# Kernel optimization log

Measured on AMD Instinct MI355X. Metric: run time of the kernel, lower is better.

## Reference

```python
import jax, jax.numpy as jnp
import numpy as np

ALPHA = 1.702
LIMIT = 7.0
BLOCK = 32  # mxfp4 block size (values per scale)

# fp4 e2m1 lookup table, indexed by 4-bit code (sign in high bit)
FP4_LUT = jnp.array([0.0, 0.5, 1.0, 1.5, 2.0, 3.0, 4.0, 6.0,
                     -0.0, -0.5, -1.0, -1.5, -2.0, -3.0, -4.0, -6.0],
                    dtype=jnp.float32)


def dequant_mxfp4(blocks, scales):
    # blocks: [E, R, C//2] int byte values (two fp4 nibbles per byte, low nibble first)
    # scales: [E, R, C//32] e8m0 exponents; value = 2^(scale - 127)
    E, R, _ = blocks.shape
    nb = scales.shape[-1]
    lo = blocks & 0xF
    hi = (blocks >> 4) & 0xF
    vals = jnp.stack([FP4_LUT[lo], FP4_LUT[hi]], axis=-1)  # [E,R,C//2,2]
    vals = vals.reshape(E, R, nb, BLOCK)
    scale = jnp.exp2((scales - 127).astype(jnp.float32))   # [E,R,nb]
    return (vals * scale[..., None]).reshape(E, R, nb * BLOCK)  # [E,R,C]


def setup_inputs() -> dict:
    key = jax.random.key(0)
    ks = jax.random.split(key, 12)
    T, E, H, I = 1024, 8, 1024, 1024
    inp = {
        'hidden_states': jax.random.normal(ks[0], (T, H), dtype=jnp.float32),
        'router_logits': jax.random.normal(ks[1], (T, E), dtype=jnp.float32),
        'gate_proj_blocks': jax.random.randint(ks[2], (E, I, H // 2), 0, 256, dtype=jnp.int32),
        'gate_proj_scales': jax.random.randint(ks[3], (E, I, H // BLOCK), 121, 130, dtype=jnp.int32),
        'gate_proj_bias': jax.random.normal(ks[4], (E, I), dtype=jnp.float32) * 0.02,
        'up_proj_blocks': jax.random.randint(ks[5], (E, I, H // 2), 0, 256, dtype=jnp.int32),
        'up_proj_scales': jax.random.randint(ks[6], (E, I, H // BLOCK), 121, 130, dtype=jnp.int32),
        'up_proj_bias': jax.random.normal(ks[7], (E, I), dtype=jnp.float32) * 0.02,
        'down_proj_blocks': jax.random.randint(ks[8], (E, H, I // 2), 0, 256, dtype=jnp.int32),
        'down_proj_scales': jax.random.randint(ks[9], (E, H, I // BLOCK), 121, 130, dtype=jnp.int32),
        'down_proj_bias': jax.random.normal(ks[10], (E, H), dtype=jnp.float32) * 0.02,
        'k': 2,
    }
    return inp


def reference(hidden_states, router_logits, gate_proj_blocks, gate_proj_scales,
              gate_proj_bias, up_proj_blocks, up_proj_scales, up_proj_bias,
              down_proj_blocks, down_proj_scales, down_proj_bias, k):
    T, H = hidden_states.shape
    E = router_logits.shape[-1]
    # --- top-k routing: softmax over the selected logits, scattered to [T,E] ---
    top_vals, top_idx = jax.lax.top_k(router_logits, k)        # [T,k]
    top_w = jax.nn.softmax(top_vals, axis=-1)                   # [T,k]
    route = jnp.zeros((T, E), dtype=hidden_states.dtype)
    route = route.at[jnp.arange(T)[:, None], top_idx].add(top_w)  # [T,E]
    # --- dequantize mxfp4 expert weights ---
    gate_w = dequant_mxfp4(gate_proj_blocks, gate_proj_scales)  # [E,I,H]
    up_w = dequant_mxfp4(up_proj_blocks, up_proj_scales)        # [E,I,H]
    down_w = dequant_mxfp4(down_proj_blocks, down_proj_scales)  # [E,H,I]
    # --- GLU expert FFN (GPT-OSS variant) ---
    gate = jnp.einsum('th,eih->tei', hidden_states, gate_w) + gate_proj_bias[None]
    up = jnp.einsum('th,eih->tei', hidden_states, up_w) + up_proj_bias[None]
    gate = jnp.minimum(gate, LIMIT)
    up = jnp.clip(up, -LIMIT, LIMIT)
    glu = gate * jax.nn.sigmoid(gate * ALPHA)
    act = (up + 1.0) * glu                                       # [T,E,I]
    # fold routing weight in before the down projection, then sum over experts
    act = act * route[:, :, None]
    out = jnp.einsum('tei,ehi->th', act, down_w) + route @ down_proj_bias  # [T,H]
    return out
```

## Files before the change

### kernel.cpp

```cpp
#include <hip/hip_runtime.h>
#include <cstdint>
#include <cstddef>

typedef __bf16 bf16x8 __attribute__((ext_vector_type(8)));
typedef __bf16 bf16x2 __attribute__((ext_vector_type(2)));
typedef float f32x16 __attribute__((ext_vector_type(16)));
typedef unsigned short u16x2 __attribute__((ext_vector_type(2)));

constexpr int HH = 1024;
constexpr int II = 1024;
constexpr int KMAX = 2;
constexpr int EMAX = 8;
constexpr int GU_TILES = 40;
constexpr int DN_TILES = 40;
constexpr float FALPHA = 1.702f;
constexpr float FLIMIT = 7.0f;

#if __has_builtin(__builtin_amdgcn_cvt_scalef32_pk_bf16_fp4)
#define USE_CVT 1
#else
#define USE_CVT 0
#endif

#define SCHED0() __builtin_amdgcn_sched_barrier(0)

__device__ __forceinline__ unsigned pk_add16(unsigned a, unsigned b) {
  u16x2 x, y;
  __builtin_memcpy(&x, &a, 4); __builtin_memcpy(&y, &b, 4);
  u16x2 r = x + y;
  unsigned o; __builtin_memcpy(&o, &r, 4); return o;
}
__device__ __forceinline__ int4 decode_chunk(int4 raw, unsigned addk) {
  unsigned p = (unsigned)raw.x | ((unsigned)raw.y << 8) |
               ((unsigned)raw.z << 16) | ((unsigned)raw.w << 24);
  unsigned q = p >> 4;
  unsigned me = p & 0x07070707u, mo = q & 0x07070707u;
  unsigned se = p & 0x08080808u, so = q & 0x08080808u;
  unsigned hiE = __builtin_amdgcn_perm(0x40404040u, 0x3F3F3F14u, me) | (se << 4);
  unsigned hiO = __builtin_amdgcn_perm(0x40404040u, 0x3F3F3F14u, mo) | (so << 4);
  unsigned loE = __builtin_amdgcn_perm(0xC0804000u, 0xC0800000u, me);
  unsigned loO = __builtin_amdgcn_perm(0xC0804000u, 0xC0800000u, mo);
  int4 out;
  out.x = (int)pk_add16(__builtin_amdgcn_perm(hiE, loE, 0x05010400u), addk);
  out.y = (int)pk_add16(__builtin_amdgcn_perm(hiE, loE, 0x07030602u), addk);
  out.z = (int)pk_add16(__builtin_amdgcn_perm(hiO, loO, 0x05010400u), addk);
  out.w = (int)pk_add16(__builtin_amdgcn_perm(hiO, loO, 0x07030602u), addk);
  return out;
}
__device__ __forceinline__ unsigned make_addk(int s) {
  int k = s - 127;
  unsigned t = ((unsigned)(k << 7)) & 0xFFFFu;
  return t | (t << 16);
}

__device__ __forceinline__ bf16x8 decode_frag(int4 raw, int s) {
#if USE_CVT
  unsigned t0 = __builtin_amdgcn_perm((unsigned)raw.y, (unsigned)raw.x, 0x00000400u);
  unsigned t1 = __builtin_amdgcn_perm((unsigned)raw.w, (unsigned)raw.z, 0x00000400u);
  unsigned p  = __builtin_amdgcn_perm(t1, t0, 0x05040100u);
  float scf = __uint_as_float((unsigned)s << 23);
  bf16x2 a = __builtin_amdgcn_cvt_scalef32_pk_bf16_fp4(p, scf, 0);
  bf16x2 b = __builtin_amdgcn_cvt_scalef32_pk_bf16_fp4(p, scf, 1);
  bf16x2 c = __builtin_amdgcn_cvt_scalef32_pk_bf16_fp4(p, scf, 2);
  bf16x2 d = __builtin_amdgcn_cvt_scalef32_pk_bf16_fp4(p, scf, 3);
  bf16x8 r;
  r[0]=a[0]; r[1]=a[1]; r[2]=b[0]; r[3]=b[1]; r[4]=c[0]; r[5]=c[1]; r[6]=d[0]; r[7]=d[1];
  return r;
#else
  int4 d4 = decode_chunk(raw, make_addk(s));
  bf16x8 r; __builtin_memcpy(&r, &d4, 16);
  return r;
#endif
}

__device__ __forceinline__ void gll16(const void* g, void* l) {
  __builtin_amdgcn_global_load_lds(
      (const __attribute__((address_space(1))) void*)g,
      (__attribute__((address_space(3))) void*)l, 16, 0, 0);
}

__device__ __forceinline__ int xcd_swz(int wg, int nwg) {
  int q = nwg >> 3, r = nwg & 7;
  int xcd = wg & 7, pos = wg >> 3;
  return (xcd < r ? xcd * (q + 1) : r * (q + 1) + (xcd - r) * q) + pos;
}

__global__ __launch_bounds__(1024) void prep_convert(
    const float* __restrict__ logits, const int* __restrict__ dk, int T, int E,
    float* __restrict__ route, float* __restrict__ tw,
    int* __restrict__ lists, int* __restrict__ counts,
    int* __restrict__ tabGU, int* __restrict__ tabDN,
    const float* __restrict__ hs, __bf16* __restrict__ hsb, int n8) {
  if ((int)blockIdx.x < (int)gridDim.x - 1) {
    int g = blockIdx.x * 1024 + threadIdx.x;
    if (g < n8) {
      const float4* p = (const float4*)hs + (size_t)g * 2;
      float4 a = p[0], b = p[1];
      bf16x8 r;
#if USE_CVT
      r[0] = (__bf16)a.x; r[1] = (__bf16)a.y; r[2] = (__bf16)a.z; r[3] = (__bf16)a.w;
      r[4] = (__bf16)b.x; r[5] = (__bf16)b.y; r[6] = (__bf16)b.z; r[7] = (__bf16)b.w;
#else
      r[0] = (__bf16)a.x; r[1] = (__bf16)a.z; r[2] = (__bf16)b.x; r[3] = (__bf16)b.z;
      r[4] = (__bf16)a.y; r[5] = (__bf16)a.w; r[6] = (__bf16)b.y; r[7] = (__bf16)b.w;
#endif
      *(bf16x8*)(hsb + (size_t)g * 8) = r;
    }
    return;
  }
  __shared__ unsigned char s_ti[1024];
  __shared__ int s_cnt[EMAX];
  int t = threadIdx.x;
  int kk = *dk; if (kk > KMAX) kk = KMAX; if (kk < 1) kk = 1;
  int EE = E > EMAX ? EMAX : E;
  if (t < T) {
    float v[EMAX]; bool used[EMAX];
    for (int e = 0; e < EE; ++e) { v[e] = logits[t * E + e]; used[e] = false; route[t * E + e] = 0.f; }
    float tv[KMAX]; int ti[KMAX];
    for (int j = 0; j < kk; ++j) {
      float best = -3.4e38f; int bi = 0;
      for (int e = 0; e < EE; ++e) if (!used[e] && v[e] > best) { best = v[e]; bi = e; }
      used[bi] = true; tv[j] = best; ti[j] = bi;
    }
    float mx = tv[0], ssum = 0.f, wj[KMAX];
    for (int j = 0; j < kk; ++j) { wj[j] = __expf(tv[j] - mx); ssum += wj[j]; }
    for (int j = 0; j < kk; ++j) {
      float wv = wj[j] / ssum;
      route[t * E + ti[j]] = wv;
      tw[t * kk + j] = wv;
    }
    s_ti[t] = (unsigned char)(ti[0] | ((kk > 1 ? ti[1] : 0xF) << 4));
  } else if (t < 1024) {
    s_ti[t] = 0xFF;
  }
  __syncthreads();
  int w = t >> 6, lane = t & 63;
  if (w < EE) {
    int e = w, cnt = 0;
    for (int base = 0; base < T; base += 64) {
      int tt = base + lane;
      int j = -1;
      if (tt < T) {
        int packed = s_ti[tt];
        if ((packed & 0xF) == e) j = 0;
        else if ((packed >> 4) == e) j = 1;
      }
      unsigned long long m = __ballot(j >= 0);
      if (j >= 0) {
        int pre = __popcll(m & ((1ull << lane) - 1ull));
        lists[e * T + cnt + pre] = (tt << 3) | j;
      }
      cnt += __popcll(m);
    }
    if (lane == 0) { counts[e] = cnt; s_cnt[e] = cnt; }
  }
  __syncthreads();
  if (t == 0) {
    int g = 0, d = 0;
    for (int e = 0; e < EE; ++e) {
      int c = s_cnt[e];
      for (int m = 0; m * 64 < c && g < GU_TILES; ++m) tabGU[g++] = (e << 16) | m;
      for (int m = 0; m * 64 < c && d < DN_TILES; ++m) tabDN[d++] = (e << 16) | m;
    }
    for (; g < GU_TILES; ++g) tabGU[g] = -1;
    for (; d < DN_TILES; ++d) tabDN[d] = -1;
  }
}

__global__ __launch_bounds__(128, 2) void gemm_gate_up(
    const __bf16* __restrict__ hsb,
    const int* __restrict__ gblk, const int* __restrict__ gscl, const float* __restrict__ gbias,
    const int* __restrict__ ublk, const int* __restrict__ uscl, const float* __restrict__ ubias,
    const int* __restrict__ lists, const int* __restrict__ counts,
    const float* __restrict__ tw, const int* __restrict__ dk,
    const int* __restrict__ tab,
    __bf16* __restrict__ act, int T)
{
  int lin = xcd_swz(blockIdx.x, GU_TILES * (II / 32));
  int ntile = lin / GU_TILES, xt = lin % GU_TILES;
  int te = tab[xt];
  if (te < 0) return;
  int e = te >> 16, mtile = te & 0xFFFF;
  int cnt = counts[e];
  int n_valid = cnt - mtile * 64;
  if (n_valid <= 0) return;
  if (n_valid > 64) n_valid = 64;
  int kk = *dk; if (kk > KMAX) kk = KMAX; if (kk < 1) kk = 1;
  int ibase = ntile * 32;

  __shared__ int s_tok[64];
  __shared__ __attribute__((aligned(16))) char Abuf[2][8192];
  __shared__ __attribute__((aligned(16))) char Bbuf[2][8192];
  __shared__ __attribute__((aligned(8))) unsigned short sS[64][36];

  int tid = threadIdx.x;
  if (tid < 64) {
    int idx = mtile * 64 + tid;
    s_tok[tid] = lists[e * T + (idx < cnt ? idx : mtile * 64)];
  }
  __syncthreads();

  int lane = tid & 63, w = tid >> 6;
  int l31 = lane & 31, kg2 = lane >> 5;
  int sub = lane >> 3, cL = lane & 7;
  int cA = cL ^ (sub & 7);

  const char* aSrc[4];
  #pragma unroll
  for (int q = 0; q < 4; ++q) {
    int row = w * 32 + q * 8 + sub;
    int tok = s_tok[row] >> 3;
    aSrc[q] = (const char*)hsb + (size_t)tok * (HH * 2) + (size_t)cA * 16;
  }
  const char* bSrc[4];
  #pragma unroll
  for (int q = 0; q < 4; ++q) {
    int row = w * 32 + q * 8 + sub;
    int mat = (row >> 4) & 1;
    int i = ibase + ((row >> 5) << 4) + (row & 15);
    const int* base = mat ? ublk : gblk;
    bSrc[q] = (const char*)(base + ((size_t)e * II + i) * (HH / 2)) + (size_t)cA * 16;
  }

  int4 sv4[4];
  #pragma unroll
  for (int rep = 0; rep < 4; ++rep) {
    int idx = tid + rep * 128;
    int row = idx >> 3, c4 = idx & 7;
    int mat = (row >> 4) & 1;
    int i = ibase + ((row >> 5) << 4) + (row & 15);
    const int* sbase = mat ? uscl : gscl;
    sv4[rep] = *((const int4*)(sbase + ((size_t)e * II + i) * 32) + c4);
  }
  asm volatile("s_waitcnt vmcnt(0)" ::: "memory");
  SCHED0();
  #pragma unroll
  for (int rep = 0; rep < 4; ++rep) {
    int idx = tid + rep * 128;
    int row = idx >> 3, c4 = idx & 7;
    unsigned short* dst = &sS[row][c4 * 4];
    dst[0] = (unsigned short)sv4[rep].x; dst[1] = (unsigned short)sv4[rep].y;
    dst[2] = (unsigned short)sv4[rep].z; dst[3] = (unsigned short)sv4[rep].w;
  }
  #pragma unroll
  for (int q = 0; q < 4; ++q) {
    gll16(aSrc[q], Abuf[0] + (w * 32 + q * 8) * 128);
    gll16(bSrc[q], Bbuf[0] + (w * 32 + q * 8) * 128);
  }
  #pragma unroll
  for (int q = 0; q < 4; ++q) {
    gll16(aSrc[q] + 128, Abuf[1] + (w * 32 + q * 8) * 128);
    gll16(bSrc[q] + 128, Bbuf[1] + (w * 32 + q * 8) * 128);
  }
  asm volatile("s_waitcnt vmcnt(8)" ::: "memory");
  asm volatile("s_waitcnt lgkmcnt(0)" ::: "memory");
  SCHED0();
  __builtin_amdgcn_s_barrier();
  SCHED0();

  f32x16 acc0 = (f32x16)0.f, acc1 = (f32x16)0.f;
  int brow = w * 32 + l31;

  constexpr int NK = HH / 64;
  #pragma unroll 1
  for (int t = 0; t < NK; ++t) {
    const char* Ac = Abuf[t & 1];
    const char* Bc = Bbuf[t & 1];
    unsigned sv = *(const unsigned*)((const char*)sS + brow * 72 + t * 4);
    #pragma unroll
    for (int s = 0; s < 4; ++s) {
      int kc = kg2 + 2 * s;
      int4 rawb = *(const int4*)(Bc + brow * 128 + ((kc ^ (brow & 7)) << 4));
      bf16x8 bb = decode_frag(rawb, (s >> 1) ? (int)(sv >> 16) : (int)(sv & 0xFFFF));
      bf16x8 a0 = *(const bf16x8*)(Ac + l31 * 128 + ((kc ^ (l31 & 7)) << 4));
      int m1 = l31 + 32;
      bf16x8 a1 = *(const bf16x8*)(Ac + m1 * 128 + ((kc ^ (m1 & 7)) << 4));
      acc0 = __builtin_amdgcn_mfma_f32_32x32x16_bf16(a0, bb, acc0, 0, 0, 0);
      acc1 = __builtin_amdgcn_mfma_f32_32x32x16_bf16(a1, bb, acc1, 0, 0, 0);
    }
    asm volatile("s_waitcnt lgkmcnt(0)" ::: "memory");
    SCHED0();
    __builtin_amdgcn_s_barrier();
    SCHED0();
    if (t + 2 < NK) {
      char* An = Abuf[t & 1];
      char* Bn = Bbuf[t & 1];
      #pragma unroll
      for (int q = 0; q < 4; ++q) {
        gll16(aSrc[q] + (t + 2) * 128, An + (w * 32 + q * 8) * 128);
        gll16(bSrc[q] + (t + 2) * 128, Bn + (w * 32 + q * 8) * 128);
      }
      asm volatile("s_waitcnt vmcnt(8)" ::: "memory");
    } else {
      asm volatile("s_waitcnt vmcnt(0)" ::: "memory");
    }
    SCHED0();
    __builtin_amdgcn_s_barrier();
    SCHED0();
  }

  {
    bool isGate = (l31 & 16) == 0;
    int i_log = ibase + w * 16 + (l31 & 15);
    float gb = gbias[e * II + i_log], ub = ubias[e * II + i_log];
#if USE_CVT
    int i_st = i_log;
#else
    int i_st = (i_log & ~7) | ((i_log & 1) << 2) | ((i_log & 7) >> 1);
#endif
    #pragma unroll
    for (int r = 0; r < 16; ++r) {
      float gv = acc0[r];
      float ov = __shfl_xor(gv, 16);
      int row = (r & 3) + 8 * (r >> 2) + 4 * kg2;
      if (isGate && row < n_valid) {
        int entry = s_tok[row];
        int t2 = entry >> 3, j = entry & 7;
        float wv = tw[t2 * kk + j];
        float g = fminf(gv + gb, FLIMIT);
        float u = fminf(fmaxf(ov + ub, -FLIMIT), FLIMIT);
        float glu = g / (1.f + __expf(-FALPHA * g));
        act[((size_t)t2 * kk + j) * II + i_st] = (__bf16)((u + 1.f) * glu * wv);
      }
    }
    #pragma unroll
    for (int r = 0; r < 16; ++r) {
      float gv = acc1[r];
      float ov = __shfl_xor(gv, 16);
      int row = (r & 3) + 8 * (r >> 2) + 4 * kg2 + 32;
      if (isGate && row < n_valid) {
        int entry = s_tok[row];
        int t2 = entry >> 3, j = entry & 7;
        float wv = tw[t2 * kk + j];
        float g = fminf(gv + gb, FLIMIT);
        float u = fminf(fmaxf(ov + ub, -FLIMIT), FLIMIT);
        float glu = g / (1.f + __expf(-FALPHA * g));
        act[((size_t)t2 * kk + j) * II + i_st] = (__bf16)((u + 1.f) * glu * wv);
      }
    }
  }
}

__global__ __launch_bounds__(128, 2) void gemm_down(
    const __bf16* __restrict__ act,
    const int* __restrict__ dblk, const int* __restrict__ dscl,
    const int* __restrict__ lists, const int* __restrict__ counts,
    const int* __restrict__ dk, const int* __restrict__ tab,
    __bf16* __restrict__ partial, int T)
{
  int lin = xcd_swz(blockIdx.x, DN_TILES * (HH / 64));
  int ntile = lin / DN_TILES, xt = lin % DN_TILES;
  int te = tab[xt];
  if (te < 0) return;
  int e = te >> 16, mtile = te & 0xFFFF;
  int cnt = counts[e];
  int n_valid = cnt - mtile * 64;
  if (n_valid <= 0) return;
  if (n_valid > 64) n_valid = 64;
  int kk = *dk; if (kk > KMAX) kk = KMAX; if (kk < 1) kk = 1;
  int hbase = ntile * 64;

  __shared__ int s_tok[64];
  __shared__ __attribute__((aligned(16))) char Abuf[2][8192];
  __shared__ __attribute__((aligned(16))) char Bbuf[2][8192];
  __shared__ __attribute__((aligned(8))) unsigned short sS[64][36];

  int tid = threadIdx.x;
  if (tid < 64) {
    int idx = mtile * 64 + tid;
    s_tok[tid] = lists[e * T + (idx < cnt ? idx : mtile * 64)];
  }
  __syncthreads();

  int lane = tid & 63, w = tid >> 6;
  int l31 = lane & 31, kg2 = lane >> 5;
  int sub = lane >> 3, cL = lane & 7;
  int cA = cL ^ (sub & 7);

  const char* aSrc[4];
  #pragma unroll
  for (int q = 0; q < 4; ++q) {
    int row = w * 32 + q * 8 + sub;
    int entry = s_tok[row];
    size_t slot = (size_t)(entry >> 3) * kk + (entry & 7);
    aSrc[q] = (const char*)act + slot * (II * 2) + (size_t)cA * 16;
  }
  const char* bSrc[4];
  #pragma unroll
  for (int q = 0; q < 4; ++q) {
    int row = w * 32 + q * 8 + sub;
    bSrc[q] = (const char*)(dblk + ((size_t)e * HH + hbase + row) * (II / 2)) + (size_t)cA * 16;
  }

  int4 sv4[4];
  #pragma unroll
  for (int rep = 0; rep < 4; ++rep) {
    int idx = tid + rep * 128;
    int row = idx >> 3, c4 = idx & 7;
    sv4[rep] = *((const int4*)(dscl + ((size_t)e * HH + hbase + row) * 32) + c4);
  }
  asm volatile("s_waitcnt vmcnt(0)" ::: "memory");
  SCHED0();
  #pragma unroll
  for (int rep = 0; rep < 4; ++rep) {
    int idx = tid + rep * 128;
    int row = idx >> 3, c4 = idx & 7;
    unsigned short* dst = &sS[row][c4 * 4];
    dst[0] = (unsigned short)sv4[rep].x; dst[1] = (unsigned short)sv4[rep].y;
    dst[2] = (unsigned short)sv4[rep].z; dst[3] = (unsigned short)sv4[rep].w;
  }
  #pragma unroll
  for (int q = 0; q < 4; ++q) {
    gll16(aSrc[q], Abuf[0] + (w * 32 + q * 8) * 128);
    gll16(bSrc[q], Bbuf[0] + (w * 32 + q * 8) * 128);
  }
  #pragma unroll
  for (int q = 0; q < 4; ++q) {
    gll16(aSrc[q] + 128, Abuf[1] + (w * 32 + q * 8) * 128);
    gll16(bSrc[q] + 128, Bbuf[1] + (w * 32 + q * 8) * 128);
  }
  asm volatile("s_waitcnt vmcnt(8)" ::: "memory");
  asm volatile("s_waitcnt lgkmcnt(0)" ::: "memory");
  SCHED0();
  __builtin_amdgcn_s_barrier();
  SCHED0();

  f32x16 acc0 = (f32x16)0.f, acc1 = (f32x16)0.f;
  int brow = w * 32 + l31;

  constexpr int NK = II / 64;
  #pragma unroll 1
  for (int t = 0; t < NK; ++t) {
    const char* Ac = Abuf[t & 1];
    const char* Bc = Bbuf[t & 1];
    unsigned sv = *(const unsigned*)((const char*)sS + brow * 72 + t * 4);
    #pragma unroll
    for (int s = 0; s < 4; ++s) {
      int kc = kg2 + 2 * s;
      int4 rawb = *(const int4*)(Bc + brow * 128 + ((kc ^ (brow & 7)) << 4));
      bf16x8 bb = decode_frag(rawb, (s >> 1) ? (int)(sv >> 16) : (int)(sv & 0xFFFF));
      bf16x8 a0 = *(const bf16x8*)(Ac + l31 * 128 + ((kc ^ (l31 & 7)) << 4));
      int m1 = l31 + 32;
      bf16x8 a1 = *(const bf16x8*)(Ac + m1 * 128 + ((kc ^ (m1 & 7)) << 4));
      acc0 = __builtin_amdgcn_mfma_f32_32x32x16_bf16(a0, bb, acc0, 0, 0, 0);
      acc1 = __builtin_amdgcn_mfma_f32_32x32x16_bf16(a1, bb, acc1, 0, 0, 0);
    }
    asm volatile("s_waitcnt lgkmcnt(0)" ::: "memory");
    SCHED0();
    __builtin_amdgcn_s_barrier();
    SCHED0();
    if (t + 2 < NK) {
      char* An = Abuf[t & 1];
      char* Bn = Bbuf[t & 1];
      #pragma unroll
      for (int q = 0; q < 4; ++q) {
        gll16(aSrc[q] + (t + 2) * 128, An + (w * 32 + q * 8) * 128);
        gll16(bSrc[q] + (t + 2) * 128, Bn + (w * 32 + q * 8) * 128);
      }
      asm volatile("s_waitcnt vmcnt(8)" ::: "memory");
    } else {
      asm volatile("s_waitcnt vmcnt(0)" ::: "memory");
    }
    SCHED0();
    __builtin_amdgcn_s_barrier();
    SCHED0();
  }

  {
    int h = hbase + w * 32 + l31;
    #pragma unroll
    for (int r = 0; r < 16; ++r) {
      int row = (r & 3) + 8 * (r >> 2) + 4 * kg2;
      if (row < n_valid) {
        int entry = s_tok[row];
        int t2 = entry >> 3, j = entry & 7;
        partial[((size_t)t2 * kk + j) * HH + h] = (__bf16)acc0[r];
      }
    }
    #pragma unroll
    for (int r = 0; r < 16; ++r) {
      int row = (r & 3) + 8 * (r >> 2) + 4 * kg2 + 32;
      if (row < n_valid) {
        int entry = s_tok[row];
        int t2 = entry >> 3, j = entry & 7;
        partial[((size_t)t2 * kk + j) * HH + h] = (__bf16)acc1[r];
      }
    }
  }
}

__global__ void combine_kernel(const __bf16* __restrict__ partial, const float* __restrict__ route,
                               const float* __restrict__ dbias, const int* __restrict__ dk,
                               float* __restrict__ out, int E) {
  int t = blockIdx.y;
  int h = blockIdx.x * 256 + threadIdx.x;
  int kk = *dk; if (kk > KMAX) kk = KMAX; if (kk < 1) kk = 1;
  float s = 0.f;
  for (int j = 0; j < kk; ++j) s += (float)partial[((size_t)t * kk + j) * HH + h];
  for (int e = 0; e < E; ++e) s += route[t * E + e] * dbias[(size_t)e * HH + h];
  out[(size_t)t * HH + h] = s;
}

extern "C" void kernel_launch(void* const* d_in, const int* in_sizes, int n_in,
                              void* d_out, int out_size, void* d_ws, size_t ws_size,
                              hipStream_t stream) {
  const float* hs    = (const float*)d_in[0];
  const float* rl    = (const float*)d_in[1];
  const int*   gblk  = (const int*)d_in[2];
  const int*   gscl  = (const int*)d_in[3];
  const float* gbias = (const float*)d_in[4];
  const int*   ublk  = (const int*)d_in[5];
  const int*   uscl  = (const int*)d_in[6];
  const float* ubias = (const float*)d_in[7];
  const int*   dblk  = (const int*)d_in[8];
  const int*   dscl  = (const int*)d_in[9];
  const float* dbias = (const float*)d_in[10];
  const int*   dk    = (const int*)d_in[11];

  long s0 = in_sizes[0], s1 = in_sizes[1], s2 = in_sizes[2], s4 = in_sizes[4];
  int H = (int)(2 * s2 / s4);
  int T = (int)(s0 / H);
  int E = (int)(s1 / T);

  char* w = (char*)d_ws;
  auto alloc = [&](size_t bytes) { char* p = w; w += (bytes + 255) & ~size_t(255); return p; };
  float*  route   = (float*)alloc(sizeof(float) * (size_t)T * E);
  float*  twp     = (float*)alloc(sizeof(float) * (size_t)T * KMAX);
  int*    counts  = (int*)  alloc(sizeof(int)   * (size_t)E);
  int*    lists   = (int*)  alloc(sizeof(int)   * (size_t)E * T);
  int*    tabGU   = (int*)  alloc(sizeof(int)   * GU_TILES);
  int*    tabDN   = (int*)  alloc(sizeof(int)   * DN_TILES);
  __bf16* hsb     = (__bf16*)alloc(sizeof(__bf16) * (size_t)T * HH);
  __bf16* act     = (__bf16*)alloc(sizeof(__bf16) * (size_t)T * KMAX * II);
  __bf16* partial = (__bf16*)alloc(sizeof(__bf16) * (size_t)T * KMAX * HH);

  int n8 = T * HH / 8;
  int nConv = (n8 + 1023) / 1024;
  prep_convert<<<dim3(nConv + 1), 1024, 0, stream>>>(
      rl, dk, T, E, route, twp, lists, counts, tabGU, tabDN, hs, hsb, n8);
  gemm_gate_up<<<dim3(GU_TILES * (II / 32)), 128, 0, stream>>>(
      hsb, gblk, gscl, gbias, ublk, uscl, ubias, lists, counts, twp, dk, tabGU, act, T);
  gemm_down<<<dim3(DN_TILES * (HH / 64)), 128, 0, stream>>>(
      act, dblk, dscl, lists, counts, dk, tabDN, partial, T);
  combine_kernel<<<dim3(HH / 256, T), 256, 0, stream>>>(partial, route, dbias, dk, (float*)d_out, E);
}
```

Measured before the change: 106.2 us.

## Enlarge MoE GEMM tiles to 8-wave blocks with 2x4 warp grid

Both expert GEMMs now run 512-thread blocks arranged as a 2x4 wave grid. Gate/up tiles grow to 128 tokens by 64 intermediate columns, and down tiles to 64 tokens by 128 hidden columns. Each loaded and dequantized weight tile is now reused across more tokens, which cuts redundant mxfp4 decode and global weight traffic. In exchange there are fewer blocks, so SM fill may suffer given roughly 2k routed tokens. LDS use per block also rises, and the larger token tiles pad more rows for experts with few tokens.

```diff
diff --git a/kernel.cpp b/kernel.cpp
--- a/kernel.cpp
+++ b/kernel.cpp
@@ -11,7 +11,7 @@
 constexpr int II = 1024;
 constexpr int KMAX = 2;
 constexpr int EMAX = 8;
-constexpr int GU_TILES = 40;
+constexpr int GU_TILES = 24;
 constexpr int DN_TILES = 40;
 constexpr float FALPHA = 1.702f;
 constexpr float FLIMIT = 7.0f;
@@ -159,7 +159,7 @@
     int g = 0, d = 0;
     for (int e = 0; e < EE; ++e) {
       int c = s_cnt[e];
-      for (int m = 0; m * 64 < c && g < GU_TILES; ++m) tabGU[g++] = (e << 16) | m;
+      for (int m = 0; m * 128 < c && g < GU_TILES; ++m) tabGU[g++] = (e << 16) | m;
       for (int m = 0; m * 64 < c && d < DN_TILES; ++m) tabDN[d++] = (e << 16) | m;
     }
     for (; g < GU_TILES; ++g) tabGU[g] = -1;
@@ -167,7 +167,7 @@
   }
 }
 
-__global__ __launch_bounds__(128, 2) void gemm_gate_up(
+__global__ __launch_bounds__(512, 2) void gemm_gate_up(
     const __bf16* __restrict__ hsb,
     const int* __restrict__ gblk, const int* __restrict__ gscl, const float* __restrict__ gbias,
     const int* __restrict__ ublk, const int* __restrict__ uscl, const float* __restrict__ ubias,
@@ -176,56 +176,57 @@
     const int* __restrict__ tab,
     __bf16* __restrict__ act, int T)
 {
-  int lin = xcd_swz(blockIdx.x, GU_TILES * (II / 32));
+  int lin = xcd_swz(blockIdx.x, GU_TILES * (II / 64));
   int ntile = lin / GU_TILES, xt = lin % GU_TILES;
   int te = tab[xt];
   if (te < 0) return;
   int e = te >> 16, mtile = te & 0xFFFF;
   int cnt = counts[e];
-  int n_valid = cnt - mtile * 64;
+  int n_valid = cnt - mtile * 128;
   if (n_valid <= 0) return;
-  if (n_valid > 64) n_valid = 64;
+  if (n_valid > 128) n_valid = 128;
   int kk = *dk; if (kk > KMAX) kk = KMAX; if (kk < 1) kk = 1;
-  int ibase = ntile * 32;
-
-  __shared__ int s_tok[64];
-  __shared__ __attribute__((aligned(16))) char Abuf[2][8192];
-  __shared__ __attribute__((aligned(16))) char Bbuf[2][8192];
-  __shared__ __attribute__((aligned(8))) unsigned short sS[64][36];
+  int ibase = ntile * 64;
+
+  __shared__ int s_tok[128];
+  __shared__ __attribute__((aligned(16))) char Abuf[2][16384];
+  __shared__ __attribute__((aligned(16))) char Bbuf[2][16384];
+  __shared__ __attribute__((aligned(8))) unsigned short sS[128][36];
 
   int tid = threadIdx.x;
-  if (tid < 64) {
-    int idx = mtile * 64 + tid;
-    s_tok[tid] = lists[e * T + (idx < cnt ? idx : mtile * 64)];
+  if (tid < 128) {
+    int idx = mtile * 128 + tid;
+    s_tok[tid] = lists[e * T + (idx < cnt ? idx : mtile * 128)];
   }
   __syncthreads();
 
   int lane = tid & 63, w = tid >> 6;
+  int wr = w >> 2, wc = w & 3;
   int l31 = lane & 31, kg2 = lane >> 5;
   int sub = lane >> 3, cL = lane & 7;
   int cA = cL ^ (sub & 7);
 
-  const char* aSrc[4];
-  #pragma unroll
-  for (int q = 0; q < 4; ++q) {
-    int row = w * 32 + q * 8 + sub;
+  const char* aSrc[2];
+  #pragma unroll
+  for (int q = 0; q < 2; ++q) {
+    int row = w * 16 + q * 8 + sub;
     int tok = s_tok[row] >> 3;
     aSrc[q] = (const char*)hsb + (size_t)tok * (HH * 2) + (size_t)cA * 16;
   }
-  const char* bSrc[4];
-  #pragma unroll
-  for (int q = 0; q < 4; ++q) {
-    int row = w * 32 + q * 8 + sub;
+  const char* bSrc[2];
+  #pragma unroll
+  for (int q = 0; q < 2; ++q) {
+    int row = w * 16 + q * 8 + sub;
     int mat = (row >> 4) & 1;
     int i = ibase + ((row >> 5) << 4) + (row & 15);
     const int* base = mat ? ublk : gblk;
     bSrc[q] = (const char*)(base + ((size_t)e * II + i) * (HH / 2)) + (size_t)cA * 16;
   }
 
-  int4 sv4[4];
-  #pragma unroll
-  for (int rep = 0; rep < 4; ++rep) {
-    int idx = tid + rep * 128;
+  int4 sv4[2];
+  #pragma unroll
+  for (int rep = 0; rep < 2; ++rep) {
+    int idx = tid + rep * 512;
     int row = idx >> 3, c4 = idx & 7;
     int mat = (row >> 4) & 1;
     int i = ibase + ((row >> 5) << 4) + (row & 15);
@@ -235,31 +236,31 @@
   asm volatile("s_waitcnt vmcnt(0)" ::: "memory");
   SCHED0();
   #pragma unroll
-  for (int rep = 0; rep < 4; ++rep) {
-    int idx = tid + rep * 128;
+  for (int rep = 0; rep < 2; ++rep) {
+    int idx = tid + rep * 512;
     int row = idx >> 3, c4 = idx & 7;
     unsigned short* dst = &sS[row][c4 * 4];
     dst[0] = (unsigned short)sv4[rep].x; dst[1] = (unsigned short)sv4[rep].y;
     dst[2] = (unsigned short)sv4[rep].z; dst[3] = (unsigned short)sv4[rep].w;
   }
   #pragma unroll
-  for (int q = 0; q < 4; ++q) {
-    gll16(aSrc[q], Abuf[0] + (w * 32 + q * 8) * 128);
-    gll16(bSrc[q], Bbuf[0] + (w * 32 + q * 8) * 128);
-  }
-  #pragma unroll
-  for (int q = 0; q < 4; ++q) {
-    gll16(aSrc[q] + 128, Abuf[1] + (w * 32 + q * 8) * 128);
-    gll16(bSrc[q] + 128, Bbuf[1] + (w * 32 + q * 8) * 128);
-  }
-  asm volatile("s_waitcnt vmcnt(8)" ::: "memory");
+  for (int q = 0; q < 2; ++q) {
+    gll16(aSrc[q], Abuf[0] + (w * 16 + q * 8) * 128);
+    gll16(bSrc[q], Bbuf[0] + (w * 16 + q * 8) * 128);
+  }
+  #pragma unroll
+  for (int q = 0; q < 2; ++q) {
+    gll16(aSrc[q] + 128, Abuf[1] + (w * 16 + q * 8) * 128);
+    gll16(bSrc[q] + 128, Bbuf[1] + (w * 16 + q * 8) * 128);
+  }
+  asm volatile("s_waitcnt vmcnt(4)" ::: "memory");
   asm volatile("s_waitcnt lgkmcnt(0)" ::: "memory");
   SCHED0();
   __builtin_amdgcn_s_barrier();
   SCHED0();
 
   f32x16 acc0 = (f32x16)0.f, acc1 = (f32x16)0.f;
-  int brow = w * 32 + l31;
+  int brow = wc * 32 + l31;
 
   constexpr int NK = HH / 64;
   #pragma unroll 1
@@ -272,8 +273,9 @@
       int kc = kg2 + 2 * s;
       int4 rawb = *(const int4*)(Bc + brow * 128 + ((kc ^ (brow & 7)) << 4));
       bf16x8 bb = decode_frag(rawb, (s >> 1) ? (int)(sv >> 16) : (int)(sv & 0xFFFF));
-      bf16x8 a0 = *(const bf16x8*)(Ac + l31 * 128 + ((kc ^ (l31 & 7)) << 4));
-      int m1 = l31 + 32;
+      int m0 = wr * 64 + l31;
+      bf16x8 a0 = *(const bf16x8*)(Ac + m0 * 128 + ((kc ^ (m0 & 7)) << 4));
+      int m1 = m0 + 32;
       bf16x8 a1 = *(const bf16x8*)(Ac + m1 * 128 + ((kc ^ (m1 & 7)) << 4));
       acc0 = __builtin_amdgcn_mfma_f32_32x32x16_bf16(a0, bb, acc0, 0, 0, 0);
       acc1 = __builtin_amdgcn_mfma_f32_32x32x16_bf16(a1, bb, acc1, 0, 0, 0);
@@ -286,11 +288,11 @@
       char* An = Abuf[t & 1];
       char* Bn = Bbuf[t & 1];
       #pragma unroll
-      for (int q = 0; q < 4; ++q) {
-        gll16(aSrc[q] + (t + 2) * 128, An + (w * 32 + q * 8) * 128);
-        gll16(bSrc[q] + (t + 2) * 128, Bn + (w * 32 + q * 8) * 128);
+      for (int q = 0; q < 2; ++q) {
+        gll16(aSrc[q] + (t + 2) * 128, An + (w * 16 + q * 8) * 128);
+        gll16(bSrc[q] + (t + 2) * 128, Bn + (w * 16 + q * 8) * 128);
       }
-      asm volatile("s_waitcnt vmcnt(8)" ::: "memory");
+      asm volatile("s_waitcnt vmcnt(4)" ::: "memory");
     } else {
       asm volatile("s_waitcnt vmcnt(0)" ::: "memory");
     }
@@ -301,7 +303,7 @@
 
   {
     bool isGate = (l31 & 16) == 0;
-    int i_log = ibase + w * 16 + (l31 & 15);
+    int i_log = ibase + wc * 16 + (l31 & 15);
     float gb = gbias[e * II + i_log], ub = ubias[e * II + i_log];
 #if USE_CVT
     int i_st = i_log;
@@ -312,7 +314,7 @@
     for (int r = 0; r < 16; ++r) {
       float gv = acc0[r];
       float ov = __shfl_xor(gv, 16);
-      int row = (r & 3) + 8 * (r >> 2) + 4 * kg2;
+      int row = wr * 64 + (r & 3) + 8 * (r >> 2) + 4 * kg2;
       if (isGate && row < n_valid) {
         int entry = s_tok[row];
         int t2 = entry >> 3, j = entry & 7;
@@ -327,7 +329,7 @@
     for (int r = 0; r < 16; ++r) {
       float gv = acc1[r];
       float ov = __shfl_xor(gv, 16);
-      int row = (r & 3) + 8 * (r >> 2) + 4 * kg2 + 32;
+      int row = wr * 64 + (r & 3) + 8 * (r >> 2) + 4 * kg2 + 32;
       if (isGate && row < n_valid) {
         int entry = s_tok[row];
         int t2 = entry >> 3, j = entry & 7;
@@ -341,14 +343,14 @@
   }
 }
 
-__global__ __launch_bounds__(128, 2) void gemm_down(
+__global__ __launch_bounds__(512, 2) void gemm_down(
     const __bf16* __restrict__ act,
     const int* __restrict__ dblk, const int* __restrict__ dscl,
     const int* __restrict__ lists, const int* __restrict__ counts,
     const int* __restrict__ dk, const int* __restrict__ tab,
     __bf16* __restrict__ partial, int T)
 {
-  int lin = xcd_swz(blockIdx.x, DN_TILES * (HH / 64));
+  int lin = xcd_swz(blockIdx.x, DN_TILES * (HH / 128));
   int ntile = lin / DN_TILES, xt = lin % DN_TILES;
   int te = tab[xt];
   if (te < 0) return;
@@ -358,12 +360,12 @@
   if (n_valid <= 0) return;
   if (n_valid > 64) n_valid = 64;
   int kk = *dk; if (kk > KMAX) kk = KMAX; if (kk < 1) kk = 1;
-  int hbase = ntile * 64;
+  int hbase = ntile * 128;
 
   __shared__ int s_tok[64];
   __shared__ __attribute__((aligned(16))) char Abuf[2][8192];
-  __shared__ __attribute__((aligned(16))) char Bbuf[2][8192];
-  __shared__ __attribute__((aligned(8))) unsigned short sS[64][36];
+  __shared__ __attribute__((aligned(16))) char Bbuf[2][16384];
+  __shared__ __attribute__((aligned(8))) unsigned short sS[128][36];
 
   int tid = threadIdx.x;
   if (tid < 64) {
@@ -373,60 +375,59 @@
   __syncthreads();
 
   int lane = tid & 63, w = tid >> 6;
+  int wr = w >> 2, wc = w & 3;
   int l31 = lane & 31, kg2 = lane >> 5;
   int sub = lane >> 3, cL = lane & 7;
   int cA = cL ^ (sub & 7);
 
-  const char* aSrc[4];
-  #pragma unroll
-  for (int q = 0; q < 4; ++q) {
-    int row = w * 32 + q * 8 + sub;
+  const char* aSrc0;
+  {
+    int row = w * 8 + sub;
     int entry = s_tok[row];
     size_t slot = (size_t)(entry >> 3) * kk + (entry & 7);
-    aSrc[q] = (const char*)act + slot * (II * 2) + (size_t)cA * 16;
-  }
-  const char* bSrc[4];
-  #pragma unroll
-  for (int q = 0; q < 4; ++q) {
-    int row = w * 32 + q * 8 + sub;
+    aSrc0 = (const char*)act + slot * (II * 2) + (size_t)cA * 16;
+  }
+  const char* bSrc[2];
+  #pragma unroll
+  for (int q = 0; q < 2; ++q) {
+    int row = w * 16 + q * 8 + sub;
     bSrc[q] = (const char*)(dblk + ((size_t)e * HH + hbase + row) * (II / 2)) + (size_t)cA * 16;
   }
 
-  int4 sv4[4];
-  #pragma unroll
-  for (int rep = 0; rep < 4; ++rep) {
-    int idx = tid + rep * 128;
+  int4 sv4[2];
+  #pragma unroll
+  for (int rep = 0; rep < 2; ++rep) {
+    int idx = tid + rep * 512;
     int row = idx >> 3, c4 = idx & 7;
     sv4[rep] = *((const int4*)(dscl + ((size_t)e * HH + hbase + row) * 32) + c4);
   }
   asm volatile("s_waitcnt vmcnt(0)" ::: "memory");
   SCHED0();
   #pragma unroll
-  for (int rep = 0; rep < 4; ++rep) {
-    int idx = tid + rep * 128;
+  for (int rep = 0; rep < 2; ++rep) {
+    int idx = tid + rep * 512;
     int row = idx >> 3, c4 = idx & 7;
     unsigned short* dst = &sS[row][c4 * 4];
     dst[0] = (unsigned short)sv4[rep].x; dst[1] = (unsigned short)sv4[rep].y;
     dst[2] = (unsigned short)sv4[rep].z; dst[3] = (unsigned short)sv4[rep].w;
   }
-  #pragma unroll
-  for (int q = 0; q < 4; ++q) {
-    gll16(aSrc[q], Abuf[0] + (w * 32 + q * 8) * 128);
-    gll16(bSrc[q], Bbuf[0] + (w * 32 + q * 8) * 128);
-  }
-  #pragma unroll
-  for (int q = 0; q < 4; ++q) {
-    gll16(aSrc[q] + 128, Abuf[1] + (w * 32 + q * 8) * 128);
-    gll16(bSrc[q] + 128, Bbuf[1] + (w * 32 + q * 8) * 128);
-  }
-  asm volatile("s_waitcnt vmcnt(8)" ::: "memory");
+  {
+    gll16(aSrc0, Abuf[0] + (w * 8) * 128);
+    #pragma unroll
+    for (int q = 0; q < 2; ++q) gll16(bSrc[q], Bbuf[0] + (w * 16 + q * 8) * 128);
+    gll16(aSrc0 + 128, Abuf[1] + (w * 8) * 128);
+    #pragma unroll
+    for (int q = 0; q < 2; ++q) gll16(bSrc[q] + 128, Bbuf[1] + (w * 16 + q * 8) * 128);
+  }
+  asm volatile("s_waitcnt vmcnt(3)" ::: "memory");
   asm volatile("s_waitcnt lgkmcnt(0)" ::: "memory");
   SCHED0();
   __builtin_amdgcn_s_barrier();
   SCHED0();
 
-  f32x16 acc0 = (f32x16)0.f, acc1 = (f32x16)0.f;
-  int brow = w * 32 + l31;
+  f32x16 acc0 = (f32x16)0.f;
+  int brow = wc * 32 + l31;
+  int m0 = wr * 32 + l31;
 
   constexpr int NK = II / 64;
   #pragma unroll 1
@@ -439,11 +440,8 @@
       int kc = kg2 + 2 * s;
       int4 rawb = *(const int4*)(Bc + brow * 128 + ((kc ^ (brow & 7)) << 4));
       bf16x8 bb = decode_frag(rawb, (s >> 1) ? (int)(sv >> 16) : (int)(sv & 0xFFFF));
-      bf16x8 a0 = *(const bf16x8*)(Ac + l31 * 128 + ((kc ^ (l31 & 7)) << 4));
-      int m1 = l31 + 32;
-      bf16x8 a1 = *(const bf16x8*)(Ac + m1 * 128 + ((kc ^ (m1 & 7)) << 4));
+      bf16x8 a0 = *(const bf16x8*)(Ac + m0 * 128 + ((kc ^ (m0 & 7)) << 4));
       acc0 = __builtin_amdgcn_mfma_f32_32x32x16_bf16(a0, bb, acc0, 0, 0, 0);
-      acc1 = __builtin_amdgcn_mfma_f32_32x32x16_bf16(a1, bb, acc1, 0, 0, 0);
     }
     asm volatile("s_waitcnt lgkmcnt(0)" ::: "memory");
     SCHED0();
@@ -452,12 +450,11 @@
     if (t + 2 < NK) {
       char* An = Abuf[t & 1];
       char* Bn = Bbuf[t & 1];
+      gll16(aSrc0 + (t + 2) * 128, An + (w * 8) * 128);
       #pragma unroll
-      for (int q = 0; q < 4; ++q) {
-        gll16(aSrc[q] + (t + 2) * 128, An + (w * 32 + q * 8) * 128);
-        gll16(bSrc[q] + (t + 2) * 128, Bn + (w * 32 + q * 8) * 128);
-      }
-      asm volatile("s_waitcnt vmcnt(8)" ::: "memory");
+      for (int q = 0; q < 2; ++q)
+        gll16(bSrc[q] + (t + 2) * 128, Bn + (w * 16 + q * 8) * 128);
+      asm volatile("s_waitcnt vmcnt(3)" ::: "memory");
     } else {
       asm volatile("s_waitcnt vmcnt(0)" ::: "memory");
     }
@@ -467,23 +464,14 @@
   }
 
   {
-    int h = hbase + w * 32 + l31;
+    int h = hbase + wc * 32 + l31;
     #pragma unroll
     for (int r = 0; r < 16; ++r) {
-      int row = (r & 3) + 8 * (r >> 2) + 4 * kg2;
+      int row = wr * 32 + (r & 3) + 8 * (r >> 2) + 4 * kg2;
       if (row < n_valid) {
         int entry = s_tok[row];
         int t2 = entry >> 3, j = entry & 7;
         partial[((size_t)t2 * kk + j) * HH + h] = (__bf16)acc0[r];
-      }
-    }
-    #pragma unroll
-    for (int r = 0; r < 16; ++r) {
-      int row = (r & 3) + 8 * (r >> 2) + 4 * kg2 + 32;
-      if (row < n_valid) {
-        int entry = s_tok[row];
-        int t2 = entry >> 3, j = entry & 7;
-        partial[((size_t)t2 * kk + j) * HH + h] = (__bf16)acc1[r];
       }
     }
   }
@@ -538,9 +526,9 @@
   int nConv = (n8 + 1023) / 1024;
   prep_convert<<<dim3(nConv + 1), 1024, 0, stream>>>(
       rl, dk, T, E, route, twp, lists, counts, tabGU, tabDN, hs, hsb, n8);
-  gemm_gate_up<<<dim3(GU_TILES * (II / 32)), 128, 0, stream>>>(
+  gemm_gate_up<<<dim3(GU_TILES * (II / 64)), 512, 0, stream>>>(
       hsb, gblk, gscl, gbias, ublk, uscl, ubias, lists, counts, twp, dk, tabGU, act, T);
-  gemm_down<<<dim3(DN_TILES * (HH / 64)), 128, 0, stream>>>(
+  gemm_down<<<dim3(DN_TILES * (HH / 128)), 512, 0, stream>>>(
       act, dblk, dscl, lists, counts, dk, tabDN, partial, T);
   combine_kernel<<<dim3(HH / 256, T), 256, 0, stream>>>(partial, route, dbias, dk, (float*)d_out, E);
 }
```

Result: faster. 96.22 us (-9.4%).
